# Optimization experiments

Hardware: AMD Instinct MI355X
Metric: run time of the kernel (lower is better)

## Reference

```python
import jax, jax.numpy as jnp
import numpy as np

BS = 16
CTX_PER = 1024   # local context nodes per proof state
ARGS_PER = 32    # arguments per proof state
KEY_DIM = 128
D_MODEL = 512


def setup_inputs() -> dict:
    key = jax.random.key(0)
    k1, k2, k3 = jax.random.split(key, 3)
    n_ctx = BS * CTX_PER
    n_args = BS * ARGS_PER
    # segment ids: sorted, uniform segments (static ragged structure)
    ctx_ids = jnp.repeat(jnp.arange(BS, dtype=jnp.int32), CTX_PER)
    arg_ids = jnp.repeat(jnp.arange(BS, dtype=jnp.int32), ARGS_PER)
    arg_values = jax.random.normal(k1, (n_args, KEY_DIM), dtype=jnp.float32)
    ctx_values = jax.random.normal(k2, (n_ctx, D_MODEL), dtype=jnp.float32)
    W = jax.random.normal(k3, (D_MODEL, KEY_DIM), dtype=jnp.float32) / np.sqrt(D_MODEL)
    b = jnp.zeros((KEY_DIM,), dtype=jnp.float32)
    return {"bs": BS, "arg_ids": arg_ids, "ctx_ids": ctx_ids,
            "arg_values": arg_values, "ctx_values": ctx_values, "W": W, "b": b}


def reference(bs, arg_ids, ctx_ids, arg_values, ctx_values, W, b):
    n_args = arg_ids.shape[0]
    n_ctx = ctx_ids.shape[0]
    # total (arg, ctx-element) pairs; static because segments are uniform by construction
    P = n_args * (n_ctx // bs)

    # ctx_lens[s] = number of context elements in proof state s
    ctx_lens = jax.ops.segment_sum(jnp.ones_like(ctx_ids), ctx_ids, num_segments=bs)
    arg_ctx_lens = ctx_lens[arg_ids]                      # [n_args]

    # ragged-range construction: row id + within-row offset for each flat pair
    arg_ends = jnp.cumsum(arg_ctx_lens)                   # inclusive cumsum
    arg_starts = arg_ends - arg_ctx_lens                  # exclusive cumsum
    pos = jnp.arange(P, dtype=arg_ends.dtype)
    rows = jnp.searchsorted(arg_ends, pos, side='right')  # value_rowids  [P]
    offs = pos - arg_starts[rows]                         # ragged range values [P]

    # column index into flat context values
    ctx_starts = jnp.cumsum(ctx_lens) - ctx_lens          # exclusive cumsum [bs]
    cols = ctx_starts[arg_ids[rows]] + offs               # [P]

    keys_all = ctx_values @ W + b                         # Dense key projection [n_ctx, key_dim]
    queries = arg_values[rows]                            # [P, key_dim]
    keys = keys_all[cols]                                 # [P, key_dim]
    logits_flat = jnp.einsum('pd,pd->p', queries, keys)   # [P]
    return rows.astype(jnp.int32), logits_flat
```

## Files before the change

kernel.cpp:

```cpp
#include <hip/hip_runtime.h>


#define BSZ        16
#define CTX_PER    1024
#define ARGS_PER   32
#define KD         128
#define DM         512
#define N_ARGS     (BSZ * ARGS_PER)
#define P_TOTAL    (N_ARGS * CTX_PER)

typedef __attribute__((ext_vector_type(8))) short short8;
typedef __attribute__((ext_vector_type(4))) float float4v;

__device__ inline short bf16_of(float x) {
    unsigned u = __builtin_bit_cast(unsigned, x);
    unsigned r = (u + 0x7fffu + ((u >> 16) & 1u)) >> 16;
    return (short)r;
}

__device__ inline short8 cvt8(float4 lo, float4 hi) {
    short8 r;
    r[0] = bf16_of(lo.x); r[1] = bf16_of(lo.y); r[2] = bf16_of(lo.z); r[3] = bf16_of(lo.w);
    r[4] = bf16_of(hi.x); r[5] = bf16_of(hi.y); r[6] = bf16_of(hi.z); r[7] = bf16_of(hi.w);
    return r;
}

__global__ __launch_bounds__(256) void qproj_kernel(
    const float* __restrict__ arg, const float* __restrict__ W,
    const float* __restrict__ b, short* __restrict__ Qp, float* __restrict__ qb)
{
    const int t = threadIdx.x, lane = t & 63, wave = t >> 6;
    const int abase = (blockIdx.x >> 2) * 16;
    const int cbase = (blockIdx.x & 3) * 128;
    const int n = lane & 15, quad = lane >> 4;

    const float* asrc = arg + (size_t)(abase + n) * KD + quad * 8;
    short8 afr[4];
    #pragma unroll
    for (int kt = 0; kt < 4; ++kt)
        afr[kt] = cvt8(*(const float4*)(asrc + kt * 32), *(const float4*)(asrc + kt * 32 + 4));

    #pragma unroll
    for (int ntl = 0; ntl < 2; ++ntl) {
        const int m = cbase + (wave * 2 + ntl) * 16 + n;
        const float* wsrc = W + (size_t)m * KD + quad * 8;
        float4v acc = {0.f, 0.f, 0.f, 0.f};
        #pragma unroll
        for (int kt = 0; kt < 4; ++kt) {
            short8 bfr = cvt8(*(const float4*)(wsrc + kt * 32), *(const float4*)(wsrc + kt * 32 + 4));
            acc = __builtin_amdgcn_mfma_f32_16x16x32_bf16(afr[kt], bfr, acc, 0, 0, 0);
        }
        #pragma unroll
        for (int r = 0; r < 4; ++r)
            Qp[(size_t)(abase + quad * 4 + r) * DM + m] = bf16_of(acc[r]);
    }

    __shared__ float red[16][17];
    const int al = t >> 4, seg = t & 15;
    const float* qrow = arg + (size_t)(abase + al) * KD + seg * 8;
    float p = 0.f;
    #pragma unroll
    for (int j = 0; j < 8; ++j) p += qrow[j] * b[seg * 8 + j];
    red[al][seg] = p;
    __syncthreads();
    if (t < 16) {
        float ssum = 0.f;
        #pragma unroll
        for (int j = 0; j < 16; ++j) ssum += red[t][j];
        qb[abase + t] = ssum;
    }
}

__global__ __launch_bounds__(256) void main_kernel(
    const float* __restrict__ ctx, const short* __restrict__ Qp,
    const float* __restrict__ qb, float* __restrict__ out)
{
    const int t = threadIdx.x, lane = t & 63, wave = t >> 6;
    const int s = blockIdx.x >> 4;
    const int chunk = blockIdx.x & 15;

    __shared__ __align__(16) short Qpl[32][520];

    {
        const short* src = Qp + (size_t)s * 32 * DM;
        #pragma unroll
        for (int i = 0; i < 8; ++i) {
            const int u = i * 256 + t;
            const int row = u >> 6, c = u & 63;
            *(float4*)&Qpl[row][c * 8] = *(const float4*)(src + (size_t)row * DM + c * 8);
        }
    }
    __syncthreads();

    const int n = lane & 15, quad = lane >> 4;
    const float* crow = ctx + (size_t)(s * CTX_PER + chunk * 64 + wave * 16 + n) * DM + quad * 8;

    float4v acc0 = {0.f, 0.f, 0.f, 0.f};
    float4v acc1 = {0.f, 0.f, 0.f, 0.f};
    #pragma unroll 4
    for (int kt = 0; kt < 16; ++kt) {
        float4 c0 = *(const float4*)(crow + kt * 32);
        float4 c1 = *(const float4*)(crow + kt * 32 + 4);
        short8 bfr = cvt8(c0, c1);
        short8 a0 = *(const short8*)&Qpl[n][kt * 32 + quad * 8];
        short8 a1 = *(const short8*)&Qpl[16 + n][kt * 32 + quad * 8];
        acc0 = __builtin_amdgcn_mfma_f32_16x16x32_bf16(a0, bfr, acc0, 0, 0, 0);
        acc1 = __builtin_amdgcn_mfma_f32_16x16x32_bf16(a1, bfr, acc1, 0, 0, 0);
    }

    const int gcol = chunk * 64 + wave * 16 + n;
    #pragma unroll
    for (int mt = 0; mt < 2; ++mt) {
        const float4v acc = mt ? acc1 : acc0;
        #pragma unroll
        for (int r = 0; r < 4; ++r) {
            const int a = s * ARGS_PER + mt * 16 + quad * 4 + r;
            out[(size_t)P_TOTAL + (size_t)a * CTX_PER + gcol] = acc[r] + qb[a];
            out[(size_t)a * CTX_PER + gcol] = (float)a;
        }
    }
}

extern "C" void kernel_launch(void* const* d_in, const int* in_sizes, int n_in,
                              void* d_out, int out_size, void* d_ws, size_t ws_size,
                              hipStream_t stream)
{
    const float* arg_values = (const float*)d_in[3];
    const float* ctx_values = (const float*)d_in[4];
    const float* W          = (const float*)d_in[5];
    const float* b          = (const float*)d_in[6];
    float* out = (float*)d_out;

    short* Qp = (short*)d_ws;
    float* qb = (float*)((char*)d_ws + (size_t)N_ARGS * DM * sizeof(short));

    qproj_kernel<<<128, 256, 0, stream>>>(arg_values, W, b, Qp, qb);
    main_kernel<<<BSZ * 16, 256, 0, stream>>>(ctx_values, Qp, qb, out);
}
```

Before: 94.18 us.

## Split main kernel K-dimension across waves and quadruple grid for more parallelism

The main kernel now assigns 16 context columns per block and splits the 512-wide reduction across four waves, combining partial sums through shared memory. The grid grows from 256 to 1024 blocks, giving more CUs and waves work so the 32MB ctx read can be better latency-hidden. Output stores become float2 vectorized. The q-projection kernel also doubles its block count with one n-tile per wave, and only one block in eight computes the bias term. The cost is that every block reloads the full 32KB Q tile into LDS, and the extra reduction adds two syncs.

```diff
diff --git a/kernel.cpp b/kernel.cpp
--- a/kernel.cpp
+++ b/kernel.cpp
@@ -30,56 +30,54 @@
     const float* __restrict__ b, short* __restrict__ Qp, float* __restrict__ qb)
 {
     const int t = threadIdx.x, lane = t & 63, wave = t >> 6;
-    const int abase = (blockIdx.x >> 2) * 16;
-    const int cbase = (blockIdx.x & 3) * 128;
+    const int mtile = blockIdx.x >> 3;
+    const int ntile = (blockIdx.x & 7) * 4 + wave;
     const int n = lane & 15, quad = lane >> 4;
 
-    const float* asrc = arg + (size_t)(abase + n) * KD + quad * 8;
+    const float* asrc = arg + (size_t)(mtile * 16 + n) * KD + quad * 8;
     short8 afr[4];
     #pragma unroll
     for (int kt = 0; kt < 4; ++kt)
         afr[kt] = cvt8(*(const float4*)(asrc + kt * 32), *(const float4*)(asrc + kt * 32 + 4));
 
+    const float* wsrc = W + (size_t)(ntile * 16 + n) * KD + quad * 8;
+    float4v acc = {0.f, 0.f, 0.f, 0.f};
     #pragma unroll
-    for (int ntl = 0; ntl < 2; ++ntl) {
-        const int m = cbase + (wave * 2 + ntl) * 16 + n;
-        const float* wsrc = W + (size_t)m * KD + quad * 8;
-        float4v acc = {0.f, 0.f, 0.f, 0.f};
+    for (int kt = 0; kt < 4; ++kt) {
+        short8 bfr = cvt8(*(const float4*)(wsrc + kt * 32), *(const float4*)(wsrc + kt * 32 + 4));
+        acc = __builtin_amdgcn_mfma_f32_16x16x32_bf16(afr[kt], bfr, acc, 0, 0, 0);
+    }
+    #pragma unroll
+    for (int r = 0; r < 4; ++r)
+        Qp[(size_t)(mtile * 16 + quad * 4 + r) * DM + ntile * 16 + n] = bf16_of(acc[r]);
+
+    if ((blockIdx.x & 7) == 0) {
+        __shared__ float red[16][17];
+        const int al = t >> 4, seg = t & 15;
+        const float* qrow = arg + (size_t)(mtile * 16 + al) * KD + seg * 8;
+        float p = 0.f;
         #pragma unroll
-        for (int kt = 0; kt < 4; ++kt) {
-            short8 bfr = cvt8(*(const float4*)(wsrc + kt * 32), *(const float4*)(wsrc + kt * 32 + 4));
-            acc = __builtin_amdgcn_mfma_f32_16x16x32_bf16(afr[kt], bfr, acc, 0, 0, 0);
+        for (int j = 0; j < 8; ++j) p += qrow[j] * b[seg * 8 + j];
+        red[al][seg] = p;
+        __syncthreads();
+        if (t < 16) {
+            float ssum = 0.f;
+            #pragma unroll
+            for (int j = 0; j < 16; ++j) ssum += red[t][j];
+            qb[mtile * 16 + t] = ssum;
         }
-        #pragma unroll
-        for (int r = 0; r < 4; ++r)
-            Qp[(size_t)(abase + quad * 4 + r) * DM + m] = bf16_of(acc[r]);
-    }
-
-    __shared__ float red[16][17];
-    const int al = t >> 4, seg = t & 15;
-    const float* qrow = arg + (size_t)(abase + al) * KD + seg * 8;
-    float p = 0.f;
-    #pragma unroll
-    for (int j = 0; j < 8; ++j) p += qrow[j] * b[seg * 8 + j];
-    red[al][seg] = p;
-    __syncthreads();
-    if (t < 16) {
-        float ssum = 0.f;
-        #pragma unroll
-        for (int j = 0; j < 16; ++j) ssum += red[t][j];
-        qb[abase + t] = ssum;
     }
 }
 
-__global__ __launch_bounds__(256) void main_kernel(
+__global__ __launch_bounds__(256, 4) void main_kernel(
     const float* __restrict__ ctx, const short* __restrict__ Qp,
     const float* __restrict__ qb, float* __restrict__ out)
 {
+    __shared__ __align__(16) short Qpl[32][520];
+
     const int t = threadIdx.x, lane = t & 63, wave = t >> 6;
-    const int s = blockIdx.x >> 4;
-    const int chunk = blockIdx.x & 15;
-
-    __shared__ __align__(16) short Qpl[32][520];
+    const int s = blockIdx.x >> 6;
+    const int chunk = blockIdx.x & 63;
 
     {
         const short* src = Qp + (size_t)s * 32 * DM;
@@ -93,32 +91,40 @@
     __syncthreads();
 
     const int n = lane & 15, quad = lane >> 4;
-    const float* crow = ctx + (size_t)(s * CTX_PER + chunk * 64 + wave * 16 + n) * DM + quad * 8;
+    const int k0 = wave * 128;
+    const float* crow = ctx + (size_t)(s * CTX_PER + chunk * 16 + n) * DM + k0 + quad * 8;
 
     float4v acc0 = {0.f, 0.f, 0.f, 0.f};
     float4v acc1 = {0.f, 0.f, 0.f, 0.f};
-    #pragma unroll 4
-    for (int kt = 0; kt < 16; ++kt) {
+    #pragma unroll
+    for (int kt = 0; kt < 4; ++kt) {
         float4 c0 = *(const float4*)(crow + kt * 32);
         float4 c1 = *(const float4*)(crow + kt * 32 + 4);
         short8 bfr = cvt8(c0, c1);
-        short8 a0 = *(const short8*)&Qpl[n][kt * 32 + quad * 8];
-        short8 a1 = *(const short8*)&Qpl[16 + n][kt * 32 + quad * 8];
+        short8 a0 = *(const short8*)&Qpl[n][k0 + kt * 32 + quad * 8];
+        short8 a1 = *(const short8*)&Qpl[16 + n][k0 + kt * 32 + quad * 8];
         acc0 = __builtin_amdgcn_mfma_f32_16x16x32_bf16(a0, bfr, acc0, 0, 0, 0);
         acc1 = __builtin_amdgcn_mfma_f32_16x16x32_bf16(a1, bfr, acc1, 0, 0, 0);
     }
 
-    const int gcol = chunk * 64 + wave * 16 + n;
+    __syncthreads();
+    float* Sp = (float*)&Qpl[0][0];
     #pragma unroll
-    for (int mt = 0; mt < 2; ++mt) {
-        const float4v acc = mt ? acc1 : acc0;
-        #pragma unroll
-        for (int r = 0; r < 4; ++r) {
-            const int a = s * ARGS_PER + mt * 16 + quad * 4 + r;
-            out[(size_t)P_TOTAL + (size_t)a * CTX_PER + gcol] = acc[r] + qb[a];
-            out[(size_t)a * CTX_PER + gcol] = (float)a;
-        }
+    for (int r = 0; r < 4; ++r) {
+        Sp[wave * 512 + (quad * 4 + r) * 16 + n]      = acc0[r];
+        Sp[wave * 512 + (16 + quad * 4 + r) * 16 + n] = acc1[r];
     }
+    __syncthreads();
+
+    const int a = t >> 3, c2 = (t & 7) * 2;
+    const int base = a * 16 + c2;
+    float v0 = Sp[base]        + Sp[512 + base]     + Sp[1024 + base]     + Sp[1536 + base];
+    float v1 = Sp[base + 1]    + Sp[512 + base + 1] + Sp[1024 + base + 1] + Sp[1536 + base + 1];
+    const int ga = s * ARGS_PER + a;
+    const float qbv = qb[ga];
+    const size_t off = (size_t)ga * CTX_PER + chunk * 16 + c2;
+    *(float2*)(out + P_TOTAL + off) = make_float2(v0 + qbv, v1 + qbv);
+    *(float2*)(out + off)           = make_float2((float)ga, (float)ga);
 }
 
 extern "C" void kernel_launch(void* const* d_in, const int* in_sizes, int n_in,
@@ -134,6 +140,6 @@
     short* Qp = (short*)d_ws;
     float* qb = (float*)((char*)d_ws + (size_t)N_ARGS * DM * sizeof(short));
 
-    qproj_kernel<<<128, 256, 0, stream>>>(arg_values, W, b, Qp, qb);
-    main_kernel<<<BSZ * 16, 256, 0, stream>>>(ctx_values, Qp, qb, out);
+    qproj_kernel<<<256, 256, 0, stream>>>(arg_values, W, b, Qp, qb);
+    main_kernel<<<BSZ * 64, 256, 0, stream>>>(ctx_values, Qp, qb, out);
 }
```

Result: no change. 94.18 us (+0.0%).
